# Kernel tuning notes

Measured on AMD Instinct MI355X. Metric: run time of the kernel, lower is better.

Reference implementation:

```python
import jax, jax.numpy as jnp
import numpy as np

B, NE, NMAX = 256, 90, 270
ZE = PE = GE = PPS = 32
NPROPS = 20
FP, SGE, LATH = 256, 64, 128
PIN = FP + SGE + LATH  # 448 = pred_inp_size = conv input (add_to_node)
C1, C2, H = 448, 256, 3
P1 = P2 = 512
EPS = 1e-5

PNAMES = ['sg_emb_table','lat_W1','lat_b1','lat_bn1_g','lat_bn1_b','lat_bn1_m','lat_bn1_v',
          'lat_W2','lat_b2','lat_bn2_g','lat_bn2_b','lat_bn2_m','lat_bn2_v',
          'z_emb_table','period_table','group_table','props','W_props','b_props','W_phys','b_phys',
          'gat1_W','gat1_as','gat1_ad','gat1_b','gat2_W','gat2_as','gat2_ad','gat2_b',
          'pW1','pb1','pbn1_g','pbn1_b','pbn1_m','pbn1_v',
          'pW2','pb2','pbn2_g','pbn2_b','pbn2_m','pbn2_v','pW3','pb3']

def _bn(x, g, b, m, v):
    return (x - m) * g / jnp.sqrt(v + EPS) + b

def _lrelu(x, s=0.2):
    return jnp.where(x >= 0, x, s * x)

def _gat(x, adj, W, a_s, a_d, bias):
    # PyG DenseGATConv: concat=False (mean over heads), dropout=0, negative_slope=0.2
    Bn, N, _ = x.shape
    h = (x @ W).reshape(Bn, N, H, -1)                      # [B,N,H,C]
    asrc = (h * a_s).sum(-1)                               # [B,N,H]
    adst = (h * a_d).sum(-1)
    alpha = asrc[:, None, :, :] + adst[:, :, None, :]      # [B,i,j,H]
    alpha = _lrelu(alpha, 0.2)
    adj_sl = jnp.maximum(adj, jnp.eye(N, dtype=adj.dtype))  # add self loops
    alpha = jnp.where(adj_sl[..., None] > 0, alpha, -jnp.inf)
    alpha = jax.nn.softmax(alpha, axis=2)                  # softmax over sources j
    out = jnp.einsum('bijh,bjhc->bihc', alpha, h)
    return out.mean(2) + bias                              # [B,N,C]

def _forward(comp, sg, lat, period_idx, group_idx, p):
    sg_x = p['sg_emb_table'][sg[:, 0]]                     # [B,SGE]
    # lattice MLP: (Linear -> BN -> LeakyReLU(True)==identity) x2
    h = _bn(lat @ p['lat_W1'] + p['lat_b1'], p['lat_bn1_g'], p['lat_bn1_b'], p['lat_bn1_m'], p['lat_bn1_v'])
    lat_x = _bn(h @ p['lat_W2'] + p['lat_b2'], p['lat_bn2_g'], p['lat_bn2_b'], p['lat_bn2_m'], p['lat_bn2_v'])
    # ragged -> dense batch: expand composition counts into dense node-type grid
    n_atoms = comp.sum(1)                                  # [B]
    cum = jnp.cumsum(comp, axis=1)                         # [B,NE]
    t = jnp.arange(NMAX)
    z = jax.vmap(lambda c: jnp.searchsorted(c, t, side='right'))(cum)  # [B,NMAX]
    mask = t[None, :] < n_atoms[:, None]                   # [B,NMAX] valid nodes
    z = jnp.where(mask, z, 0)
    # PhysEmbedding: z/period/group embeddings + projected properties -> final proj
    phys = jnp.concatenate([
        p['z_emb_table'][z],
        p['period_table'][period_idx[z]],
        p['group_table'][group_idx[z]],
        p['props'][z] @ p['W_props'] + p['b_props'],
    ], axis=-1)
    phys = phys @ p['W_phys'] + p['b_phys']                # [B,NMAX,FP]
    # add_to_node: cat graph-level lat/sg embeddings onto every node, then zero-pad
    node = jnp.concatenate([
        phys,
        jnp.broadcast_to(lat_x[:, None, :], (lat_x.shape[0], NMAX, LATH)),
        jnp.broadcast_to(sg_x[:, None, :], (sg_x.shape[0], NMAX, SGE)),
    ], axis=-1)
    node = node * mask[..., None].astype(node.dtype)       # to_dense_batch zero padding
    # per-graph dense block adjacency, zero diagonal (fill_diagonal_(0))
    adj = (mask[:, :, None] & mask[:, None, :]).astype(node.dtype)
    adj = adj * (1.0 - jnp.eye(NMAX, dtype=node.dtype))
    # GNNBlock: act = LeakyReLU(True) == identity (negative_slope=1)
    x1 = _gat(node, adj, p['gat1_W'], p['gat1_as'], p['gat1_ad'], p['gat1_b'])
    x2 = _gat(x1, adj, p['gat2_W'], p['gat2_as'], p['gat2_ad'], p['gat2_b'])
    comp_x = x2.sum(1)                                     # sum over ALL NMAX slots (incl. padding, as torch does)
    feat = jnp.concatenate([comp_x, sg_x, lat_x], axis=-1) # [B,PIN]
    # prediction head (eval: dropout off, BN running stats)
    h = _lrelu(_bn(feat @ p['pW1'] + p['pb1'], p['pbn1_g'], p['pbn1_b'], p['pbn1_m'], p['pbn1_v']))
    h = _lrelu(_bn(h @ p['pW2'] + p['pb2'], p['pbn2_g'], p['pbn2_b'], p['pbn2_m'], p['pbn2_v']))
    return h @ p['pW3'] + p['pb3']                         # [B,1]

def setup_inputs():
    key = jax.random.key(0)
    ks = iter(jax.random.split(key, 64))
    def nrm(shape, s=0.05):
        return jax.random.normal(next(ks), shape, dtype=jnp.float32) * s
    comp = jax.random.randint(next(ks), (B, NE), 0, 4, dtype=jnp.int32)
    comp = comp.at[0].set(3)  # graph 0 has exactly NMAX atoms -> data N_max == NMAX
    sg = jax.random.randint(next(ks), (B, 1), 0, 230)
    lat = jax.random.uniform(next(ks), (B, 6), dtype=jnp.float32)
    period_idx = jax.random.randint(next(ks), (NE,), 0, 8)
    group_idx = jax.random.randint(next(ks), (NE,), 0, 19)
    inp = dict(comp=comp, sg=sg, lat=lat, period_idx=period_idx, group_idx=group_idx)
    inp.update(
        sg_emb_table=nrm((230, SGE)),
        lat_W1=nrm((6, LATH)), lat_b1=nrm((LATH,)),
        lat_bn1_g=jnp.ones(LATH), lat_bn1_b=jnp.zeros(LATH), lat_bn1_m=jnp.zeros(LATH), lat_bn1_v=jnp.ones(LATH),
        lat_W2=nrm((LATH, LATH)), lat_b2=nrm((LATH,)),
        lat_bn2_g=jnp.ones(LATH), lat_bn2_b=jnp.zeros(LATH), lat_bn2_m=jnp.zeros(LATH), lat_bn2_v=jnp.ones(LATH),
        z_emb_table=nrm((NE, ZE)), period_table=nrm((8, PE)), group_table=nrm((19, GE)),
        props=nrm((NE, NPROPS), 0.1), W_props=nrm((NPROPS, PPS)), b_props=nrm((PPS,)),
        W_phys=nrm((ZE + PE + GE + PPS, FP)), b_phys=nrm((FP,)),
        gat1_W=nrm((PIN, H * C1)), gat1_as=nrm((H, C1)), gat1_ad=nrm((H, C1)), gat1_b=nrm((C1,)),
        gat2_W=nrm((C1, H * C2)), gat2_as=nrm((H, C2)), gat2_ad=nrm((H, C2)), gat2_b=nrm((C2,)),
        pW1=nrm((PIN, P1)), pb1=nrm((P1,)),
        pbn1_g=jnp.ones(P1), pbn1_b=jnp.zeros(P1), pbn1_m=jnp.zeros(P1), pbn1_v=jnp.ones(P1),
        pW2=nrm((P1, P2)), pb2=nrm((P2,)),
        pbn2_g=jnp.ones(P2), pbn2_b=jnp.zeros(P2), pbn2_m=jnp.zeros(P2), pbn2_v=jnp.ones(P2),
        pW3=nrm((P2, 1)), pb3=nrm((1,)),
    )
    return inp

def reference(comp, sg, lat, period_idx, group_idx,
              sg_emb_table, lat_W1, lat_b1, lat_bn1_g, lat_bn1_b, lat_bn1_m, lat_bn1_v,
              lat_W2, lat_b2, lat_bn2_g, lat_bn2_b, lat_bn2_m, lat_bn2_v,
              z_emb_table, period_table, group_table, props, W_props, b_props, W_phys, b_phys,
              gat1_W, gat1_as, gat1_ad, gat1_b, gat2_W, gat2_as, gat2_ad, gat2_b,
              pW1, pb1, pbn1_g, pbn1_b, pbn1_m, pbn1_v,
              pW2, pb2, pbn2_g, pbn2_b, pbn2_m, pbn2_v, pW3, pb3):
    vals = (sg_emb_table, lat_W1, lat_b1, lat_bn1_g, lat_bn1_b, lat_bn1_m, lat_bn1_v,
            lat_W2, lat_b2, lat_bn2_g, lat_bn2_b, lat_bn2_m, lat_bn2_v,
            z_emb_table, period_table, group_table, props, W_props, b_props, W_phys, b_phys,
            gat1_W, gat1_as, gat1_ad, gat1_b, gat2_W, gat2_as, gat2_ad, gat2_b,
            pW1, pb1, pbn1_g, pbn1_b, pbn1_m, pbn1_v,
            pW2, pb2, pbn2_g, pbn2_b, pbn2_m, pbn2_v, pW3, pb3)
    p = dict(zip(PNAMES, vals))
    return _forward(comp, sg, lat, period_idx, group_idx, p)
```

## Files before the change

kernel.cpp:

```cpp
#include <hip/hip_runtime.h>
#include <math.h>

#define BB 256
#define NEL 90
#define NMAX 270
#define C1 448
#define C2 256
#define PIN 448
#define LATH 128
#define SGE 64
#define P1 512
#define EPSB 1e-5f

typedef short shortx8 __attribute__((ext_vector_type(8)));
typedef float floatx4 __attribute__((ext_vector_type(4)));

__device__ __forceinline__ float bf2f(unsigned short u) {
  return __uint_as_float(((unsigned)u) << 16);
}
__device__ __forceinline__ unsigned short f2bf(float f) {
  unsigned x = __float_as_uint(f);
  unsigned r = (x + 0x7fffu + ((x >> 16) & 1u)) >> 16;
  return (unsigned short)r;
}
__device__ __forceinline__ void gld16(const void* g, void* l) {
  __builtin_amdgcn_global_load_lds(
      (const __attribute__((address_space(1))) unsigned int*)g,
      (__attribute__((address_space(3))) unsigned int*)l, 16, 0, 0);
}

#define NB_PREP  BB
#define NB_SCAN  1
#define NB_PHYS  NEL
#define NB_WP1   (14 * 42)
#define NB_WP2   (14 * 24)
#define NB_FOLD  112
#define NB_PAD   64
#define SETUP_GRID (NB_PREP + NB_SCAN + NB_PHYS + NB_WP1 + NB_WP2 + 2 * NB_FOLD + NB_PAD)

__global__ __launch_bounds__(256) void k_setup(
    const int* __restrict__ comp, const int* __restrict__ sg, const float* __restrict__ lat,
    const float* __restrict__ sg_emb,
    const float* __restrict__ lW1, const float* __restrict__ lb1,
    const float* __restrict__ lg1, const float* __restrict__ lbe1,
    const float* __restrict__ lm1, const float* __restrict__ lv1,
    const float* __restrict__ lW2, const float* __restrict__ lb2,
    const float* __restrict__ lg2, const float* __restrict__ lbe2,
    const float* __restrict__ lm2, const float* __restrict__ lv2,
    const int* __restrict__ period_idx, const int* __restrict__ group_idx,
    const float* __restrict__ z_emb, const float* __restrict__ period_t,
    const float* __restrict__ group_t, const float* __restrict__ props,
    const float* __restrict__ Wp, const float* __restrict__ bp,
    const float* __restrict__ Wphys, const float* __restrict__ bphys,
    const float* __restrict__ gat1_W, const float* __restrict__ gat1_as,
    const float* __restrict__ gat1_ad, const float* __restrict__ gat1_b,
    const float* __restrict__ gat2_W, const float* __restrict__ gat2_as,
    const float* __restrict__ gat2_ad, const float* __restrict__ gat2_b,
    float* __restrict__ sgx, float* __restrict__ latx, int* __restrict__ z,
    int* __restrict__ natoms, int* __restrict__ off, int* __restrict__ aoff,
    float* __restrict__ zerobuf, float* __restrict__ physpe,
    unsigned short* __restrict__ wt1, unsigned short* __restrict__ wt2,
    float* __restrict__ wsv1, float* __restrict__ wdv1,
    float* __restrict__ wsv2, float* __restrict__ wdv2, float* __restrict__ pad2) {
  int r = blockIdx.x;
  int tid = threadIdx.x;
  int wv = tid >> 6, lane = tid & 63;

  if (r < NB_PREP) {
    int b = r;
    __shared__ int cum[NEL];
    __shared__ float hbuf[LATH];
    __shared__ float latl[6];
    if (tid == 0) {
      int s = 0;
      for (int e = 0; e < NEL; ++e) { s += comp[b * NEL + e]; cum[e] = s; }
    }
    if (tid < 6) latl[tid] = lat[b * 6 + tid];
    __syncthreads();
    int n = cum[NEL - 1];
    for (int t = tid; t < NMAX; t += 256) {
      int zz = -1;
      if (t < n) {
        for (int e = 0; e < NEL; ++e) { if (cum[e] > t) { zz = e; break; } }
      }
      z[b * NMAX + t] = zz;
    }
    if (tid < SGE) sgx[b * SGE + tid] = sg_emb[sg[b] * SGE + tid];
    if (tid < LATH) {
      float acc = lb1[tid];
      for (int k = 0; k < 6; ++k) acc += latl[k] * lW1[k * LATH + tid];
      acc = (acc - lm1[tid]) * lg1[tid] * rsqrtf(lv1[tid] + EPSB) + lbe1[tid];
      hbuf[tid] = acc;
    }
    __syncthreads();
    if (tid < LATH) {
      float acc = lb2[tid];
      for (int k = 0; k < LATH; ++k) acc += hbuf[k] * lW2[k * LATH + tid];
      acc = (acc - lm2[tid]) * lg2[tid] * rsqrtf(lv2[tid] + EPSB) + lbe2[tid];
      latx[b * LATH + tid] = acc;
    }
    return;
  }
  r -= NB_PREP;
  if (r < NB_SCAN) {
    __shared__ int sh[BB];
    zerobuf[tid] = 0.f;
    int v0 = 0;
    for (int e = 0; e < NEL; ++e) v0 += comp[tid * NEL + e];
    natoms[tid] = v0;
    sh[tid] = v0;
    for (int d = 1; d < BB; d <<= 1) {
      __syncthreads();
      int v = (tid >= d) ? sh[tid - d] : 0;
      __syncthreads();
      sh[tid] += v;
    }
    __syncthreads();
    off[tid] = sh[tid] - v0;
    __syncthreads();
    int sz = 3 * ((((v0 + 15) >> 4) << 4)) * ((((v0 + 31) >> 5) << 5));
    sh[tid] = sz;
    for (int d = 1; d < BB; d <<= 1) {
      __syncthreads();
      int v = (tid >= d) ? sh[tid - d] : 0;
      __syncthreads();
      sh[tid] += v;
    }
    __syncthreads();
    aoff[tid] = sh[tid] - sz;
    return;
  }
  r -= NB_SCAN;
  if (r < NB_PHYS) {
    int e = r;
    __shared__ float ph[128];
    if (tid < 32) ph[tid] = z_emb[e * 32 + tid];
    else if (tid < 64) ph[tid] = period_t[period_idx[e] * 32 + tid - 32];
    else if (tid < 96) ph[tid] = group_t[group_idx[e] * 32 + tid - 64];
    else if (tid < 128) {
      int j = tid - 96;
      float acc = bp[j];
      for (int k = 0; k < 20; ++k) acc += props[e * 20 + k] * Wp[k * 32 + j];
      ph[tid] = acc;
    }
    __syncthreads();
    float acc = bphys[tid];
    for (int k = 0; k < 128; ++k) acc += ph[k] * Wphys[k * 256 + tid];
    physpe[e * 256 + tid] = acc;
    return;
  }
  r -= NB_PHYS;
  if (r < NB_WP1 + NB_WP2) {
    const float* W;
    unsigned short* Wt;
    int NC3, bx, by;
    if (r < NB_WP1) { W = gat1_W; Wt = wt1; NC3 = 3 * C1; bx = r % 14; by = r / 14; }
    else { int r2 = r - NB_WP1; W = gat2_W; Wt = wt2; NC3 = 3 * C2; bx = r2 % 14; by = r2 / 14; }
    int k0 = bx << 5, c0 = by << 5;
    __shared__ float ts[32][33];
    int e4 = tid << 2;
    int kk = e4 >> 5, cc = e4 & 31;
    float4 v = *(const float4*)(W + (size_t)(k0 + kk) * NC3 + c0 + cc);
    ts[kk][cc] = v.x; ts[kk][cc + 1] = v.y; ts[kk][cc + 2] = v.z; ts[kk][cc + 3] = v.w;
    __syncthreads();
    int c2 = tid & 31, kg = tid >> 5;
    ushort4 u;
    u.x = f2bf(ts[kg * 4 + 0][c2]); u.y = f2bf(ts[kg * 4 + 1][c2]);
    u.z = f2bf(ts[kg * 4 + 2][c2]); u.w = f2bf(ts[kg * 4 + 3][c2]);
    *(ushort4*)(Wt + (size_t)(c0 + c2) * 448 + k0 + (kg << 2)) = u;
    return;
  }
  r -= NB_WP1 + NB_WP2;
  if (r < 2 * NB_FOLD) {
    const float* W; const float* as_; const float* ad_;
    float* wsv; float* wdv; int NC3, C, kb;
    if (r < NB_FOLD) { W = gat1_W; as_ = gat1_as; ad_ = gat1_ad; wsv = wsv1; wdv = wdv1; NC3 = 3 * C1; C = C1; kb = r << 2; }
    else { int r2 = r - NB_FOLD; W = gat2_W; as_ = gat2_as; ad_ = gat2_ad; wsv = wsv2; wdv = wdv2; NC3 = 3 * C2; C = C2; kb = r2 << 2; }
    int k = kb + wv;
    for (int h = 0; h < 3; ++h) {
      float ss = 0.f, sd = 0.f;
      for (int c = lane; c < C; c += 64) {
        float wvv = W[(size_t)k * NC3 + h * C + c];
        ss += wvv * as_[h * C + c];
        sd += wvv * ad_[h * C + c];
      }
      for (int o = 32; o > 0; o >>= 1) { ss += __shfl_xor(ss, o); sd += __shfl_xor(sd, o); }
      if (lane == 0) { wsv[k * 3 + h] = ss; wdv[k * 3 + h] = sd; }
    }
    return;
  }
  r -= 2 * NB_FOLD;
  {
    int c = (r << 2) + wv;
    float s = 0.f;
    for (int k = lane; k < C1; k += 64) {
      const float* wr = gat2_W + (size_t)k * (3 * C2) + c;
      s += gat1_b[k] * (wr[0] + wr[C2] + wr[2 * C2]);
    }
    for (int o = 32; o > 0; o >>= 1) s += __shfl_xor(s, o);
    if (lane == 0) pad2[c] = s * (1.f / 3.f) + gat2_b[c];
  }
}

__global__ __launch_bounds__(256) void k_nodep(
    const int* __restrict__ z, const int* __restrict__ off, const int* __restrict__ natoms,
    const float* __restrict__ physpe, const float* __restrict__ latx,
    const float* __restrict__ sgx, unsigned short* __restrict__ x0) {
  int b = blockIdx.x;
  int n = natoms[b], ob = off[b];
  int tid = threadIdx.x;
  __shared__ int zl[NMAX];
  for (int t = tid; t < n; t += 256) zl[t] = z[b * NMAX + t];
  __syncthreads();
  int items = n * 56;
  for (int e = tid; e < items; e += 256) {
    int t = e / 56, c8 = (e - t * 56) << 3;
    int zt = zl[t];
    float v[8];
    if (c8 < 256) {
      float4 a = *(const float4*)(physpe + zt * 256 + c8);
      float4 c = *(const float4*)(physpe + zt * 256 + c8 + 4);
      v[0] = a.x; v[1] = a.y; v[2] = a.z; v[3] = a.w;
      v[4] = c.x; v[5] = c.y; v[6] = c.z; v[7] = c.w;
    } else if (c8 < 384) {
      float4 a = *(const float4*)(latx + b * LATH + c8 - 256);
      float4 c = *(const float4*)(latx + b * LATH + c8 - 252);
      v[0] = a.x; v[1] = a.y; v[2] = a.z; v[3] = a.w;
      v[4] = c.x; v[5] = c.y; v[6] = c.z; v[7] = c.w;
    } else {
      float4 a = *(const float4*)(sgx + b * SGE + c8 - 384);
      float4 c = *(const float4*)(sgx + b * SGE + c8 - 380);
      v[0] = a.x; v[1] = a.y; v[2] = a.z; v[3] = a.w;
      v[4] = c.x; v[5] = c.y; v[6] = c.z; v[7] = c.w;
    }
    unsigned short u[8];
    #pragma unroll
    for (int i = 0; i < 8; ++i) u[i] = f2bf(v[i]);
    *(uint4*)(x0 + (size_t)(ob + t) * PIN + c8) = *(uint4*)u;
  }
}

__global__ __launch_bounds__(256) void k_av2(
    const unsigned short* __restrict__ x, const float* __restrict__ wsv,
    const float* __restrict__ wdv, const int* __restrict__ off,
    const int* __restrict__ natoms, float* __restrict__ asrc,
    float* __restrict__ adst, int K) {
  __shared__ float sw[C1 * 3], dw[C1 * 3];
  int tid = threadIdx.x;
  for (int e = tid; e < K * 3; e += 256) { sw[e] = wsv[e]; dw[e] = wdv[e]; }
  __syncthreads();
  int total = off[BB - 1] + natoms[BB - 1];
  int wv = tid >> 6, lane = tid & 63;
  int nk8 = K >> 3;
  int stride = gridDim.x << 2;
  for (int row = (blockIdx.x << 2) + wv; row < total; row += stride) {
    float s0 = 0.f, s1 = 0.f, s2 = 0.f, d0 = 0.f, d1 = 0.f, d2 = 0.f;
    if (lane < nk8) {
      uint4 raw = *(const uint4*)(x + (size_t)row * K + (lane << 3));
      unsigned short us[8];
      *(uint4*)us = raw;
      #pragma unroll
      for (int u = 0; u < 8; ++u) {
        float xv = bf2f(us[u]);
        int kb = ((lane << 3) + u) * 3;
        s0 += xv * sw[kb + 0]; s1 += xv * sw[kb + 1]; s2 += xv * sw[kb + 2];
        d0 += xv * dw[kb + 0]; d1 += xv * dw[kb + 1]; d2 += xv * dw[kb + 2];
      }
    }
    #pragma unroll
    for (int o = 32; o > 0; o >>= 1) {
      s0 += __shfl_xor(s0, o); s1 += __shfl_xor(s1, o); s2 += __shfl_xor(s2, o);
      d0 += __shfl_xor(d0, o); d1 += __shfl_xor(d1, o); d2 += __shfl_xor(d2, o);
    }
    if (lane == 0) {
      asrc[row * 3 + 0] = s0; asrc[row * 3 + 1] = s1; asrc[row * 3 + 2] = s2;
      adst[row * 3 + 0] = d0; adst[row * 3 + 1] = d1; adst[row * 3 + 2] = d2;
    }
  }
}

#define MTMAX 17
__global__ __launch_bounds__(256) void k_alpha(
    const float* __restrict__ asrc, const float* __restrict__ adst,
    const int* __restrict__ off, const int* __restrict__ natoms,
    const int* __restrict__ aoff, unsigned short* __restrict__ alpha) {
  int bid = blockIdx.x;
  int b = bid & (BB - 1);
  int hm = bid >> 8;
  int h = hm % 3;
  int mt = hm / 3;
  int n = natoms[b];
  if (n == 0) return;
  int mtn = (n + 15) >> 4;
  if (mt >= mtn) return;
  int ktn = (n + 31) >> 5;
  int rext = mtn << 4, kext = ktn << 5;
  int ob = off[b];
  size_t ab = (size_t)aoff[b] + (size_t)h * rext * kext;
  int tid = threadIdx.x;
  int wv = tid >> 6, lane = tid & 63;
  __shared__ float asl[288];
  for (int j = tid; j < kext; j += 256)
    asl[j] = (j < n) ? asrc[(ob + j) * 3 + h] : 0.f;
  __syncthreads();
  #pragma unroll
  for (int r = 0; r < 4; ++r) {
    int i = (mt << 4) + (wv << 2) + r;
    unsigned short* rowp = alpha + ab + (size_t)i * kext;
    if (i >= n) {
      for (int j = lane; j < kext; j += 64) rowp[j] = 0;
      continue;
    }
    float ad = adst[(ob + i) * 3 + h];
    float m = -1e30f;
    for (int j = lane; j < n; j += 64) {
      float sc = asl[j] + ad;
      sc = fmaxf(sc, 0.2f * sc);
      m = fmaxf(m, sc);
    }
    for (int o = 32; o > 0; o >>= 1) m = fmaxf(m, __shfl_xor(m, o));
    float s = 0.f;
    for (int j = lane; j < n; j += 64) {
      float sc = asl[j] + ad;
      sc = fmaxf(sc, 0.2f * sc);
      s += __expf(sc - m);
    }
    for (int o = 32; o > 0; o >>= 1) s += __shfl_xor(s, o);
    float rs = 1.f / s;
    for (int j = lane; j < kext; j += 64) {
      float v = 0.f;
      if (j < n) {
        float sc = asl[j] + ad;
        sc = fmaxf(sc, 0.2f * sc);
        v = __expf(sc - m) * rs;
      }
      rowp[j] = f2bf(v);
    }
  }
}

#define MTW 5

__global__ __launch_bounds__(256, 2) void k_fused_mfma(
    const unsigned short* __restrict__ xin, const unsigned short* __restrict__ Wt,
    const unsigned short* __restrict__ alpha, const int* __restrict__ aoff,
    const int* __restrict__ off, const int* __restrict__ natoms,
    const float* __restrict__ bias, const float* __restrict__ zerobuf,
    unsigned short* __restrict__ xout, int K, int C, int NC) {
  int bid = blockIdx.x;
  int xg = bid & 7;
  int g = bid >> 3;
  int cblk = g % NC;
  int b = xg + ((g / NC) << 3);
  int c0 = cblk << 6;
  int n = natoms[b];
  if (n == 0) return;
  int ob = off[b];
  size_t ab = (size_t)aoff[b];
  int tid = threadIdx.x;
  int wv = tid >> 6;
  int lane = tid & 63;
  int m16 = lane & 15;
  int q = lane >> 4;

  int mtn = (n + 15) >> 4;
  int jmax = mtn << 4;
  int ktn = (n + 31) >> 5;
  int kext = ktn << 5;
  size_t hstride = (size_t)jmax * kext;

  __shared__ unsigned short xs[2][17 * 512];
  __shared__ unsigned short tt[36 * 512];

  const unsigned short* xsrc[MTW];
  #pragma unroll
  for (int t_i = 0; t_i < MTW; ++t_i) {
    int mt = wv + (t_i << 2);
    int j = (mt << 4) + m16;
    xsrc[t_i] = (j < n) ? (xin + (size_t)(ob + j) * K + (q << 3))
                        : (const unsigned short*)zerobuf;
  }

  floatx4 acc[MTW][4];
  #pragma unroll
  for (int i = 0; i < MTW; ++i)
    #pragma unroll
    for (int nt = 0; nt < 4; ++nt) acc[i][nt] = (floatx4)0.f;

  for (int h = 0; h < 3; ++h) {
    floatx4 tac[MTW][4];
    #pragma unroll
    for (int i = 0; i < MTW; ++i)
      #pragma unroll
      for (int nt = 0; nt < 4; ++nt) tac[i][nt] = (floatx4)0.f;

    const unsigned short* wsrc = Wt + (size_t)(h * C + c0 + lane) * K + (wv << 3);

    #pragma unroll
    for (int t_i = 0; t_i < MTW; ++t_i) {
      int mt = wv + (t_i << 2);
      if (mt < mtn) gld16(xsrc[t_i], &xs[0][mt << 9]);
    }
    gld16(wsrc, &tt[wv << 9]);
    __syncthreads();

    int buf = 0;
    for (int k0 = 0; k0 < K; k0 += 32) {
      int k1 = k0 + 32;
      if (k1 < K) {
        #pragma unroll
        for (int t_i = 0; t_i < MTW; ++t_i) {
          int mt = wv + (t_i << 2);
          if (mt < mtn) gld16(xsrc[t_i] + k1, &xs[buf ^ 1][mt << 9]);
        }
        gld16(wsrc + k1, &tt[((buf ^ 1) << 11) + (wv << 9)]);
      }
      const unsigned short* wb = &tt[buf << 11];
      shortx8 bfr[4];
      #pragma unroll
      for (int nt = 0; nt < 4; ++nt)
        bfr[nt] = *(const shortx8*)(wb + (q << 9) + (((nt << 4) + m16) << 3));
      #pragma unroll
      for (int t_i = 0; t_i < MTW; ++t_i) {
        int mt = wv + (t_i << 2);
        if (mt < mtn) {
          shortx8 a = *(const shortx8*)(&xs[buf][(mt << 9) + (((q << 4) + m16) << 3)]);
          #pragma unroll
          for (int nt = 0; nt < 4; ++nt)
            tac[t_i][nt] = __builtin_amdgcn_mfma_f32_16x16x32_bf16(a, bfr[nt], tac[t_i][nt], 0, 0, 0);
        }
      }
      __syncthreads();
      buf ^= 1;
    }
    #pragma unroll
    for (int t_i = 0; t_i < MTW; ++t_i) {
      int mt = wv + (t_i << 2);
      if (mt < mtn) {
        int jbase = (mt << 4) + (q << 2);
        #pragma unroll
        for (int nt = 0; nt < 4; ++nt) {
          floatx4 d = tac[t_i][nt];
          ushort4 u;
          u.x = f2bf(d.x); u.y = f2bf(d.y); u.z = f2bf(d.z); u.w = f2bf(d.w);
          int c = (nt << 4) + m16;
          *(ushort4*)(tt + ((jbase >> 3) << 9) + (c << 3) + (jbase & 7)) = u;
        }
      }
    }
    for (int e = tid; e < ((kext - jmax) << 6); e += 256) {
      int j = jmax + (e >> 6), c = e & 63;
      tt[((j >> 3) << 9) + (c << 3) + (j & 7)] = 0;
    }
    __syncthreads();
    const unsigned short* ap = alpha + ab + (size_t)h * hstride;
    for (int k0p = 0; k0p < kext; k0p += 32) {
      shortx8 tb[4];
      #pragma unroll
      for (int nt = 0; nt < 4; ++nt)
        tb[nt] = *(const shortx8*)(tt + (((k0p >> 3) + q) << 9) + (((nt << 4) + m16) << 3));
      #pragma unroll
      for (int t_i = 0; t_i < MTW; ++t_i) {
        int mt = wv + (t_i << 2);
        if (mt < mtn) {
          shortx8 af = *(const shortx8*)(ap + (size_t)((mt << 4) + m16) * kext + k0p + (q << 3));
          #pragma unroll
          for (int nt = 0; nt < 4; ++nt)
            acc[t_i][nt] = __builtin_amdgcn_mfma_f32_16x16x32_bf16(af, tb[nt], acc[t_i][nt], 0, 0, 0);
        }
      }
    }
    __syncthreads();
  }
  float bq[4];
  #pragma unroll
  for (int nt = 0; nt < 4; ++nt) bq[nt] = bias[c0 + (nt << 4) + m16];
  const float inv3 = 1.f / 3.f;
  #pragma unroll
  for (int t_i = 0; t_i < MTW; ++t_i) {
    int mt = wv + (t_i << 2);
    if (mt < mtn) {
      #pragma unroll
      for (int nt = 0; nt < 4; ++nt) {
        floatx4 d = acc[t_i][nt];
        int cidx = c0 + (nt << 4) + m16;
        #pragma unroll
        for (int r = 0; r < 4; ++r) {
          int i = (mt << 4) + (q << 2) + r;
          if (i < n) xout[(size_t)(ob + i) * C + cidx] = f2bf(d[r] * inv3 + bq[nt]);
        }
      }
    }
  }
}

__global__ __launch_bounds__(256) void k_feat2(
    const unsigned short* __restrict__ x2, const float* __restrict__ pad2,
    const int* __restrict__ off, const int* __restrict__ natoms,
    const float* __restrict__ sgx, const float* __restrict__ latx,
    float* __restrict__ feat) {
  int b = blockIdx.y;
  int chunk = blockIdx.x;
  int tid = threadIdx.x;
  int n = natoms[b], ob = off[b];
  if (chunk == 17) {
    atomicAdd(&feat[b * PIN + tid], (float)(NMAX - n) * pad2[tid]);
    if (tid < SGE) feat[b * PIN + 256 + tid] = sgx[b * SGE + tid];
    if (tid < LATH) feat[b * PIN + 320 + tid] = latx[b * LATH + tid];
    return;
  }
  int i0 = chunk << 4;
  if (i0 >= n) return;
  int i1 = min(i0 + 16, n);
  float s = 0.f;
  for (int i = i0; i < i1; ++i) s += bf2f(x2[(size_t)(ob + i) * C2 + tid]);
  atomicAdd(&feat[b * PIN + tid], s);
}

__global__ __launch_bounds__(512) void k_head(
    const float* __restrict__ feat,
    const float* __restrict__ W1, const float* __restrict__ b1,
    const float* __restrict__ g1, const float* __restrict__ be1,
    const float* __restrict__ m1, const float* __restrict__ v1,
    const float* __restrict__ W2, const float* __restrict__ b2,
    const float* __restrict__ g2, const float* __restrict__ be2,
    const float* __restrict__ m2, const float* __restrict__ v2,
    const float* __restrict__ W3, const float* __restrict__ b3,
    float* __restrict__ out) {
  int b = blockIdx.x, tid = threadIdx.x;
  __shared__ float f[PIN];
  __shared__ float h1[P1];
  __shared__ float h2[P1];
  __shared__ float red[512];
  for (int i = tid; i < PIN; i += 512) f[i] = feat[b * PIN + i];
  __syncthreads();
  {
    int o = tid;
    float acc = b1[o];
    for (int k = 0; k < PIN; ++k) acc += f[k] * W1[k * P1 + o];
    acc = (acc - m1[o]) * g1[o] * rsqrtf(v1[o] + EPSB) + be1[o];
    h1[o] = acc >= 0.f ? acc : 0.2f * acc;
  }
  __syncthreads();
  {
    int o = tid;
    float acc = b2[o];
    for (int k = 0; k < P1; ++k) acc += h1[k] * W2[k * P1 + o];
    acc = (acc - m2[o]) * g2[o] * rsqrtf(v2[o] + EPSB) + be2[o];
    h2[o] = acc >= 0.f ? acc : 0.2f * acc;
  }
  __syncthreads();
  red[tid] = h2[tid] * W3[tid];
  __syncthreads();
  for (int s = 256; s > 0; s >>= 1) {
    if (tid < s) red[tid] += red[tid + s];
    __syncthreads();
  }
  if (tid == 0) out[b] = red[0] + b3[0];
}

extern "C" void kernel_launch(void* const* d_in, const int* in_sizes, int n_in,
                              void* d_out, int out_size, void* d_ws, size_t ws_size,
                              hipStream_t stream) {
  const int*   comp       = (const int*)d_in[0];
  const int*   sg         = (const int*)d_in[1];
  const float* lat        = (const float*)d_in[2];
  const int*   period_idx = (const int*)d_in[3];
  const int*   group_idx  = (const int*)d_in[4];
  const float* sg_emb     = (const float*)d_in[5];
  const float* lat_W1     = (const float*)d_in[6];
  const float* lat_b1     = (const float*)d_in[7];
  const float* lat_bn1_g  = (const float*)d_in[8];
  const float* lat_bn1_b  = (const float*)d_in[9];
  const float* lat_bn1_m  = (const float*)d_in[10];
  const float* lat_bn1_v  = (const float*)d_in[11];
  const float* lat_W2     = (const float*)d_in[12];
  const float* lat_b2     = (const float*)d_in[13];
  const float* lat_bn2_g  = (const float*)d_in[14];
  const float* lat_bn2_b  = (const float*)d_in[15];
  const float* lat_bn2_m  = (const float*)d_in[16];
  const float* lat_bn2_v  = (const float*)d_in[17];
  const float* z_emb      = (const float*)d_in[18];
  const float* period_t   = (const float*)d_in[19];
  const float* group_t    = (const float*)d_in[20];
  const float* props      = (const float*)d_in[21];
  const float* W_props    = (const float*)d_in[22];
  const float* b_props    = (const float*)d_in[23];
  const float* W_phys     = (const float*)d_in[24];
  const float* b_phys     = (const float*)d_in[25];
  const float* gat1_W     = (const float*)d_in[26];
  const float* gat1_as    = (const float*)d_in[27];
  const float* gat1_ad    = (const float*)d_in[28];
  const float* gat1_b     = (const float*)d_in[29];
  const float* gat2_W     = (const float*)d_in[30];
  const float* gat2_as    = (const float*)d_in[31];
  const float* gat2_ad    = (const float*)d_in[32];
  const float* gat2_b     = (const float*)d_in[33];
  const float* pW1        = (const float*)d_in[34];
  const float* pb1        = (const float*)d_in[35];
  const float* pbn1_g     = (const float*)d_in[36];
  const float* pbn1_b     = (const float*)d_in[37];
  const float* pbn1_m     = (const float*)d_in[38];
  const float* pbn1_v     = (const float*)d_in[39];
  const float* pW2        = (const float*)d_in[40];
  const float* pb2        = (const float*)d_in[41];
  const float* pbn2_g     = (const float*)d_in[42];
  const float* pbn2_b     = (const float*)d_in[43];
  const float* pbn2_m     = (const float*)d_in[44];
  const float* pbn2_v     = (const float*)d_in[45];
  const float* pW3        = (const float*)d_in[46];
  const float* pb3        = (const float*)d_in[47];

  float* ws = (float*)d_ws;
  const size_t o_sgx  = 0;
  const size_t o_latx = o_sgx  + (size_t)BB * SGE;
  const size_t o_nat  = o_latx + (size_t)BB * LATH;
  const size_t o_off  = o_nat  + BB;
  const size_t o_aoff = o_off  + BB;
  const size_t o_z    = o_aoff + BB;
  const size_t o_phys = o_z    + (size_t)BB * NMAX;
  const size_t o_wsv1 = o_phys + (size_t)NEL * 256;
  const size_t o_wdv1 = o_wsv1 + (size_t)C1 * 3;
  const size_t o_wsv2 = o_wdv1 + (size_t)C1 * 3;
  const size_t o_wdv2 = o_wsv2 + (size_t)C1 * 3;
  const size_t o_asrc = o_wdv2 + (size_t)C1 * 3;
  const size_t o_adst = o_asrc + (size_t)BB * NMAX * 3;
  const size_t o_pad2 = o_adst + (size_t)BB * NMAX * 3;
  const size_t o_zero = o_pad2 + 256;
  const size_t o_wt1  = o_zero + 256;
  const size_t o_wt2  = o_wt1  + (size_t)(3 * C1) * PIN / 2;
  const size_t o_x0   = o_wt2  + (size_t)(3 * C2) * C1 / 2;
  const size_t o_x1   = o_x0   + (size_t)BB * NMAX * PIN / 2;
  const size_t o_alph = o_x1   + (size_t)BB * NMAX * PIN / 2;

  float* sgx    = ws + o_sgx;
  float* latx   = ws + o_latx;
  int*   natoms = (int*)(ws + o_nat);
  int*   off    = (int*)(ws + o_off);
  int*   aoff   = (int*)(ws + o_aoff);
  int*   z      = (int*)(ws + o_z);
  float* physpe = ws + o_phys;
  float* wsv1   = ws + o_wsv1;
  float* wdv1   = ws + o_wdv1;
  float* wsv2   = ws + o_wsv2;
  float* wdv2   = ws + o_wdv2;
  float* asrc   = ws + o_asrc;
  float* adst   = ws + o_adst;
  float* pad2   = ws + o_pad2;
  float* zerobuf = ws + o_zero;
  unsigned short* wt1   = (unsigned short*)(ws + o_wt1);
  unsigned short* wt2   = (unsigned short*)(ws + o_wt2);
  unsigned short* x0    = (unsigned short*)(ws + o_x0);
  unsigned short* x1    = (unsigned short*)(ws + o_x1);
  unsigned short* x2    = x0;
  unsigned short* alpha = (unsigned short*)(ws + o_alph);
  float* feat   = ws + o_x1;

  const int ALG = BB * 3 * MTMAX;

  k_setup<<<SETUP_GRID, 256, 0, stream>>>(
      comp, sg, lat, sg_emb,
      lat_W1, lat_b1, lat_bn1_g, lat_bn1_b, lat_bn1_m, lat_bn1_v,
      lat_W2, lat_b2, lat_bn2_g, lat_bn2_b, lat_bn2_m, lat_bn2_v,
      period_idx, group_idx, z_emb, period_t, group_t, props,
      W_props, b_props, W_phys, b_phys,
      gat1_W, gat1_as, gat1_ad, gat1_b,
      gat2_W, gat2_as, gat2_ad, gat2_b,
      sgx, latx, z, natoms, off, aoff, zerobuf, physpe,
      wt1, wt2, wsv1, wdv1, wsv2, wdv2, pad2);

  k_nodep<<<BB, 256, 0, stream>>>(z, off, natoms, physpe, latx, sgx, x0);

  k_av2<<<1024, 256, 0, stream>>>(x0, wsv1, wdv1, off, natoms, asrc, adst, PIN);
  k_alpha<<<ALG, 256, 0, stream>>>(asrc, adst, off, natoms, aoff, alpha);
  k_fused_mfma<<<(C1 / 64) * BB, 256, 0, stream>>>(x0, wt1, alpha, aoff,
      off, natoms, gat1_b, zerobuf, x1, PIN, C1, C1 / 64);

  k_av2<<<1024, 256, 0, stream>>>(x1, wsv2, wdv2, off, natoms, asrc, adst, C1);
  k_alpha<<<ALG, 256, 0, stream>>>(asrc, adst, off, natoms, aoff, alpha);
  k_fused_mfma<<<(C2 / 64) * BB, 256, 0, stream>>>(x1, wt2, alpha, aoff,
      off, natoms, gat2_b, zerobuf, x2, C1, C2, C2 / 64);

  hipMemsetAsync(feat, 0, (size_t)BB * PIN * sizeof(float), stream);
  k_feat2<<<dim3(18, BB), 256, 0, stream>>>(x2, pad2, off, natoms, sgx, latx, feat);
  k_head<<<BB, 512, 0, stream>>>(feat,
      pW1, pb1, pbn1_g, pbn1_b, pbn1_m, pbn1_v,
      pW2, pb2, pbn2_g, pbn2_b, pbn2_m, pbn2_v,
      pW3, pb3, (float*)d_out);
}
```

Baseline: 747.0 us.

## Fuse node build, attention scores and softmax per graph; fuse pooling into head

Node feature construction, the attention-vector dot products and the softmax alpha computation are merged into one per-graph kernel that keeps asrc/adst in shared memory. The same merge is done for layer two. Feature pooling is folded into the MLP head, which removes the memset, the atomics and the feat buffer. Launches and global round-trips go down, but each stage now runs on only 256 blocks, so GPU occupancy is lower. Layer one's attention scores now use the fp32 features instead of the bf16-rounded ones.

```diff
diff --git a/kernel.cpp b/kernel.cpp
--- a/kernel.cpp
+++ b/kernel.cpp
@@ -202,126 +202,29 @@
   }
 }
 
-__global__ __launch_bounds__(256) void k_nodep(
-    const int* __restrict__ z, const int* __restrict__ off, const int* __restrict__ natoms,
-    const float* __restrict__ physpe, const float* __restrict__ latx,
-    const float* __restrict__ sgx, unsigned short* __restrict__ x0) {
-  int b = blockIdx.x;
-  int n = natoms[b], ob = off[b];
-  int tid = threadIdx.x;
-  __shared__ int zl[NMAX];
-  for (int t = tid; t < n; t += 256) zl[t] = z[b * NMAX + t];
-  __syncthreads();
-  int items = n * 56;
-  for (int e = tid; e < items; e += 256) {
-    int t = e / 56, c8 = (e - t * 56) << 3;
-    int zt = zl[t];
-    float v[8];
-    if (c8 < 256) {
-      float4 a = *(const float4*)(physpe + zt * 256 + c8);
-      float4 c = *(const float4*)(physpe + zt * 256 + c8 + 4);
-      v[0] = a.x; v[1] = a.y; v[2] = a.z; v[3] = a.w;
-      v[4] = c.x; v[5] = c.y; v[6] = c.z; v[7] = c.w;
-    } else if (c8 < 384) {
-      float4 a = *(const float4*)(latx + b * LATH + c8 - 256);
-      float4 c = *(const float4*)(latx + b * LATH + c8 - 252);
-      v[0] = a.x; v[1] = a.y; v[2] = a.z; v[3] = a.w;
-      v[4] = c.x; v[5] = c.y; v[6] = c.z; v[7] = c.w;
-    } else {
-      float4 a = *(const float4*)(sgx + b * SGE + c8 - 384);
-      float4 c = *(const float4*)(sgx + b * SGE + c8 - 380);
-      v[0] = a.x; v[1] = a.y; v[2] = a.z; v[3] = a.w;
-      v[4] = c.x; v[5] = c.y; v[6] = c.z; v[7] = c.w;
-    }
-    unsigned short u[8];
-    #pragma unroll
-    for (int i = 0; i < 8; ++i) u[i] = f2bf(v[i]);
-    *(uint4*)(x0 + (size_t)(ob + t) * PIN + c8) = *(uint4*)u;
-  }
-}
-
-__global__ __launch_bounds__(256) void k_av2(
-    const unsigned short* __restrict__ x, const float* __restrict__ wsv,
-    const float* __restrict__ wdv, const int* __restrict__ off,
-    const int* __restrict__ natoms, float* __restrict__ asrc,
-    float* __restrict__ adst, int K) {
-  __shared__ float sw[C1 * 3], dw[C1 * 3];
-  int tid = threadIdx.x;
-  for (int e = tid; e < K * 3; e += 256) { sw[e] = wsv[e]; dw[e] = wdv[e]; }
-  __syncthreads();
-  int total = off[BB - 1] + natoms[BB - 1];
-  int wv = tid >> 6, lane = tid & 63;
-  int nk8 = K >> 3;
-  int stride = gridDim.x << 2;
-  for (int row = (blockIdx.x << 2) + wv; row < total; row += stride) {
-    float s0 = 0.f, s1 = 0.f, s2 = 0.f, d0 = 0.f, d1 = 0.f, d2 = 0.f;
-    if (lane < nk8) {
-      uint4 raw = *(const uint4*)(x + (size_t)row * K + (lane << 3));
-      unsigned short us[8];
-      *(uint4*)us = raw;
-      #pragma unroll
-      for (int u = 0; u < 8; ++u) {
-        float xv = bf2f(us[u]);
-        int kb = ((lane << 3) + u) * 3;
-        s0 += xv * sw[kb + 0]; s1 += xv * sw[kb + 1]; s2 += xv * sw[kb + 2];
-        d0 += xv * dw[kb + 0]; d1 += xv * dw[kb + 1]; d2 += xv * dw[kb + 2];
-      }
-    }
-    #pragma unroll
-    for (int o = 32; o > 0; o >>= 1) {
-      s0 += __shfl_xor(s0, o); s1 += __shfl_xor(s1, o); s2 += __shfl_xor(s2, o);
-      d0 += __shfl_xor(d0, o); d1 += __shfl_xor(d1, o); d2 += __shfl_xor(d2, o);
-    }
-    if (lane == 0) {
-      asrc[row * 3 + 0] = s0; asrc[row * 3 + 1] = s1; asrc[row * 3 + 2] = s2;
-      adst[row * 3 + 0] = d0; adst[row * 3 + 1] = d1; adst[row * 3 + 2] = d2;
-    }
-  }
-}
-
-#define MTMAX 17
-__global__ __launch_bounds__(256) void k_alpha(
-    const float* __restrict__ asrc, const float* __restrict__ adst,
-    const int* __restrict__ off, const int* __restrict__ natoms,
-    const int* __restrict__ aoff, unsigned short* __restrict__ alpha) {
-  int bid = blockIdx.x;
-  int b = bid & (BB - 1);
-  int hm = bid >> 8;
-  int h = hm % 3;
-  int mt = hm / 3;
-  int n = natoms[b];
-  if (n == 0) return;
-  int mtn = (n + 15) >> 4;
-  if (mt >= mtn) return;
-  int ktn = (n + 31) >> 5;
-  int rext = mtn << 4, kext = ktn << 5;
-  int ob = off[b];
-  size_t ab = (size_t)aoff[b] + (size_t)h * rext * kext;
-  int tid = threadIdx.x;
-  int wv = tid >> 6, lane = tid & 63;
-  __shared__ float asl[288];
-  for (int j = tid; j < kext; j += 256)
-    asl[j] = (j < n) ? asrc[(ob + j) * 3 + h] : 0.f;
-  __syncthreads();
-  #pragma unroll
-  for (int r = 0; r < 4; ++r) {
-    int i = (mt << 4) + (wv << 2) + r;
-    unsigned short* rowp = alpha + ab + (size_t)i * kext;
+__device__ __forceinline__ void alpha_phase(
+    const float* asl, const float* adl, unsigned short* __restrict__ alpha,
+    size_t ab, int n, int rext, int kext, int wv8, int lane) {
+  for (int hr = wv8; hr < 3 * rext; hr += 8) {
+    int h = (hr >= 2 * rext) ? 2 : (hr >= rext ? 1 : 0);
+    int i = hr - h * rext;
+    unsigned short* rowp = alpha + ab + (size_t)h * rext * kext + (size_t)i * kext;
     if (i >= n) {
       for (int j = lane; j < kext; j += 64) rowp[j] = 0;
       continue;
     }
-    float ad = adst[(ob + i) * 3 + h];
+    const float* asp = asl + h * 288;
+    float ad = adl[h * 288 + i];
     float m = -1e30f;
     for (int j = lane; j < n; j += 64) {
-      float sc = asl[j] + ad;
+      float sc = asp[j] + ad;
       sc = fmaxf(sc, 0.2f * sc);
       m = fmaxf(m, sc);
     }
     for (int o = 32; o > 0; o >>= 1) m = fmaxf(m, __shfl_xor(m, o));
     float s = 0.f;
     for (int j = lane; j < n; j += 64) {
-      float sc = asl[j] + ad;
+      float sc = asp[j] + ad;
       sc = fmaxf(sc, 0.2f * sc);
       s += __expf(sc - m);
     }
@@ -330,13 +233,128 @@
     for (int j = lane; j < kext; j += 64) {
       float v = 0.f;
       if (j < n) {
-        float sc = asl[j] + ad;
+        float sc = asp[j] + ad;
         sc = fmaxf(sc, 0.2f * sc);
         v = __expf(sc - m) * rs;
       }
       rowp[j] = f2bf(v);
     }
   }
+}
+
+__global__ __launch_bounds__(512) void k_node_avalpha(
+    const int* __restrict__ z, const int* __restrict__ off, const int* __restrict__ natoms,
+    const float* __restrict__ physpe, const float* __restrict__ latx,
+    const float* __restrict__ sgx, const float* __restrict__ wsv,
+    const float* __restrict__ wdv, const int* __restrict__ aoff,
+    unsigned short* __restrict__ x0, unsigned short* __restrict__ alpha) {
+  int b = blockIdx.x;
+  int n = natoms[b];
+  if (n == 0) return;
+  int ob = off[b];
+  int tid = threadIdx.x;
+  int wv8 = tid >> 6, lane = tid & 63;
+  __shared__ int zl[NMAX];
+  __shared__ float wsl[PIN * 3], wdl[PIN * 3];
+  __shared__ float asl[3 * 288], adl[3 * 288];
+  for (int t = tid; t < n; t += 512) zl[t] = z[b * NMAX + t];
+  for (int e = tid; e < PIN * 3; e += 512) { wsl[e] = wsv[e]; wdl[e] = wdv[e]; }
+  for (int e = tid; e < 3 * 288; e += 512) { asl[e] = 0.f; adl[e] = 0.f; }
+  __syncthreads();
+  int mtn = (n + 15) >> 4, ktn = (n + 31) >> 5;
+  int rext = mtn << 4, kext = ktn << 5;
+  for (int r = wv8; r < n; r += 8) {
+    int zt = zl[r];
+    float s0 = 0.f, s1 = 0.f, s2 = 0.f, d0 = 0.f, d1 = 0.f, d2 = 0.f;
+    if (lane < 56) {
+      int c8 = lane << 3;
+      float v[8];
+      if (c8 < 256) {
+        float4 a = *(const float4*)(physpe + zt * 256 + c8);
+        float4 c = *(const float4*)(physpe + zt * 256 + c8 + 4);
+        v[0] = a.x; v[1] = a.y; v[2] = a.z; v[3] = a.w;
+        v[4] = c.x; v[5] = c.y; v[6] = c.z; v[7] = c.w;
+      } else if (c8 < 384) {
+        float4 a = *(const float4*)(latx + b * LATH + c8 - 256);
+        float4 c = *(const float4*)(latx + b * LATH + c8 - 252);
+        v[0] = a.x; v[1] = a.y; v[2] = a.z; v[3] = a.w;
+        v[4] = c.x; v[5] = c.y; v[6] = c.z; v[7] = c.w;
+      } else {
+        float4 a = *(const float4*)(sgx + b * SGE + c8 - 384);
+        float4 c = *(const float4*)(sgx + b * SGE + c8 - 380);
+        v[0] = a.x; v[1] = a.y; v[2] = a.z; v[3] = a.w;
+        v[4] = c.x; v[5] = c.y; v[6] = c.z; v[7] = c.w;
+      }
+      unsigned short u[8];
+      #pragma unroll
+      for (int i = 0; i < 8; ++i) u[i] = f2bf(v[i]);
+      *(uint4*)(x0 + (size_t)(ob + r) * PIN + c8) = *(uint4*)u;
+      #pragma unroll
+      for (int i = 0; i < 8; ++i) {
+        int kb = (c8 + i) * 3;
+        s0 += v[i] * wsl[kb + 0]; s1 += v[i] * wsl[kb + 1]; s2 += v[i] * wsl[kb + 2];
+        d0 += v[i] * wdl[kb + 0]; d1 += v[i] * wdl[kb + 1]; d2 += v[i] * wdl[kb + 2];
+      }
+    }
+    #pragma unroll
+    for (int o = 32; o > 0; o >>= 1) {
+      s0 += __shfl_xor(s0, o); s1 += __shfl_xor(s1, o); s2 += __shfl_xor(s2, o);
+      d0 += __shfl_xor(d0, o); d1 += __shfl_xor(d1, o); d2 += __shfl_xor(d2, o);
+    }
+    if (lane == 0) {
+      asl[0 * 288 + r] = s0; asl[1 * 288 + r] = s1; asl[2 * 288 + r] = s2;
+      adl[0 * 288 + r] = d0; adl[1 * 288 + r] = d1; adl[2 * 288 + r] = d2;
+    }
+  }
+  __syncthreads();
+  alpha_phase(asl, adl, alpha, (size_t)aoff[b], n, rext, kext, wv8, lane);
+}
+
+__global__ __launch_bounds__(512) void k_avalpha(
+    const unsigned short* __restrict__ x, const float* __restrict__ wsv,
+    const float* __restrict__ wdv, const int* __restrict__ off,
+    const int* __restrict__ natoms, const int* __restrict__ aoff,
+    unsigned short* __restrict__ alpha) {
+  int b = blockIdx.x;
+  int n = natoms[b];
+  if (n == 0) return;
+  int ob = off[b];
+  int tid = threadIdx.x;
+  int wv8 = tid >> 6, lane = tid & 63;
+  __shared__ float wsl[C1 * 3], wdl[C1 * 3];
+  __shared__ float asl[3 * 288], adl[3 * 288];
+  for (int e = tid; e < C1 * 3; e += 512) { wsl[e] = wsv[e]; wdl[e] = wdv[e]; }
+  for (int e = tid; e < 3 * 288; e += 512) { asl[e] = 0.f; adl[e] = 0.f; }
+  __syncthreads();
+  int mtn = (n + 15) >> 4, ktn = (n + 31) >> 5;
+  int rext = mtn << 4, kext = ktn << 5;
+  for (int r = wv8; r < n; r += 8) {
+    float s0 = 0.f, s1 = 0.f, s2 = 0.f, d0 = 0.f, d1 = 0.f, d2 = 0.f;
+    if (lane < 56) {
+      int c8 = lane << 3;
+      uint4 raw = *(const uint4*)(x + (size_t)(ob + r) * C1 + c8);
+      unsigned short us[8];
+      *(uint4*)us = raw;
+      #pragma unroll
+      for (int i = 0; i < 8; ++i) {
+        float v = bf2f(us[i]);
+        int kb = (c8 + i) * 3;
+        s0 += v * wsl[kb + 0]; s1 += v * wsl[kb + 1]; s2 += v * wsl[kb + 2];
+        d0 += v * wdl[kb + 0]; d1 += v * wdl[kb + 1]; d2 += v * wdl[kb + 2];
+      }
+    }
+    #pragma unroll
+    for (int o = 32; o > 0; o >>= 1) {
+      s0 += __shfl_xor(s0, o); s1 += __shfl_xor(s1, o); s2 += __shfl_xor(s2, o);
+      d0 += __shfl_xor(d0, o); d1 += __shfl_xor(d1, o); d2 += __shfl_xor(d2, o);
+    }
+    if (lane == 0) {
+      asl[0 * 288 + r] = s0; asl[1 * 288 + r] = s1; asl[2 * 288 + r] = s2;
+      adl[0 * 288 + r] = d0; adl[1 * 288 + r] = d1; adl[2 * 288 + r] = d2;
+    }
+  }
+  __syncthreads();
+  alpha_phase(asl, adl, alpha, (size_t)aoff[b], n, rext, kext, wv8, lane);
 }
 
 #define MTW 5
@@ -494,31 +512,10 @@
   }
 }
 
-__global__ __launch_bounds__(256) void k_feat2(
+__global__ __launch_bounds__(512) void k_feat_head(
     const unsigned short* __restrict__ x2, const float* __restrict__ pad2,
     const int* __restrict__ off, const int* __restrict__ natoms,
     const float* __restrict__ sgx, const float* __restrict__ latx,
-    float* __restrict__ feat) {
-  int b = blockIdx.y;
-  int chunk = blockIdx.x;
-  int tid = threadIdx.x;
-  int n = natoms[b], ob = off[b];
-  if (chunk == 17) {
-    atomicAdd(&feat[b * PIN + tid], (float)(NMAX - n) * pad2[tid]);
-    if (tid < SGE) feat[b * PIN + 256 + tid] = sgx[b * SGE + tid];
-    if (tid < LATH) feat[b * PIN + 320 + tid] = latx[b * LATH + tid];
-    return;
-  }
-  int i0 = chunk << 4;
-  if (i0 >= n) return;
-  int i1 = min(i0 + 16, n);
-  float s = 0.f;
-  for (int i = i0; i < i1; ++i) s += bf2f(x2[(size_t)(ob + i) * C2 + tid]);
-  atomicAdd(&feat[b * PIN + tid], s);
-}
-
-__global__ __launch_bounds__(512) void k_head(
-    const float* __restrict__ feat,
     const float* __restrict__ W1, const float* __restrict__ b1,
     const float* __restrict__ g1, const float* __restrict__ be1,
     const float* __restrict__ m1, const float* __restrict__ v1,
@@ -528,11 +525,35 @@
     const float* __restrict__ W3, const float* __restrict__ b3,
     float* __restrict__ out) {
   int b = blockIdx.x, tid = threadIdx.x;
+  int wv8 = tid >> 6, lane = tid & 63;
+  int n = natoms[b], ob = off[b];
+  __shared__ float part[8][256];
   __shared__ float f[PIN];
   __shared__ float h1[P1];
   __shared__ float h2[P1];
   __shared__ float red[512];
-  for (int i = tid; i < PIN; i += 512) f[i] = feat[b * PIN + i];
+  float a0 = 0.f, a1 = 0.f, a2 = 0.f, a3 = 0.f;
+  for (int r = wv8; r < n; r += 8) {
+    uint2 raw = *(const uint2*)(x2 + (size_t)(ob + r) * C2 + (lane << 2));
+    unsigned short us[4];
+    *(uint2*)us = raw;
+    a0 += bf2f(us[0]); a1 += bf2f(us[1]); a2 += bf2f(us[2]); a3 += bf2f(us[3]);
+  }
+  {
+    float4 p = make_float4(a0, a1, a2, a3);
+    *(float4*)&part[wv8][lane << 2] = p;
+  }
+  __syncthreads();
+  if (tid < 256) {
+    float s = 0.f;
+    #pragma unroll
+    for (int w = 0; w < 8; ++w) s += part[w][tid];
+    f[tid] = s + (float)(NMAX - n) * pad2[tid];
+  } else if (tid < 320) {
+    f[tid] = sgx[b * SGE + (tid - 256)];
+  } else if (tid < 448) {
+    f[tid] = latx[b * LATH + (tid - 320)];
+  }
   __syncthreads();
   {
     int o = tid;
@@ -623,9 +644,7 @@
   const size_t o_wdv1 = o_wsv1 + (size_t)C1 * 3;
   const size_t o_wsv2 = o_wdv1 + (size_t)C1 * 3;
   const size_t o_wdv2 = o_wsv2 + (size_t)C1 * 3;
-  const size_t o_asrc = o_wdv2 + (size_t)C1 * 3;
-  const size_t o_adst = o_asrc + (size_t)BB * NMAX * 3;
-  const size_t o_pad2 = o_adst + (size_t)BB * NMAX * 3;
+  const size_t o_pad2 = o_wdv2 + (size_t)C1 * 3;
   const size_t o_zero = o_pad2 + 256;
   const size_t o_wt1  = o_zero + 256;
   const size_t o_wt2  = o_wt1  + (size_t)(3 * C1) * PIN / 2;
@@ -644,8 +663,6 @@
   float* wdv1   = ws + o_wdv1;
   float* wsv2   = ws + o_wsv2;
   float* wdv2   = ws + o_wdv2;
-  float* asrc   = ws + o_asrc;
-  float* adst   = ws + o_adst;
   float* pad2   = ws + o_pad2;
   float* zerobuf = ws + o_zero;
   unsigned short* wt1   = (unsigned short*)(ws + o_wt1);
@@ -654,9 +671,6 @@
   unsigned short* x1    = (unsigned short*)(ws + o_x1);
   unsigned short* x2    = x0;
   unsigned short* alpha = (unsigned short*)(ws + o_alph);
-  float* feat   = ws + o_x1;
-
-  const int ALG = BB * 3 * MTMAX;
 
   k_setup<<<SETUP_GRID, 256, 0, stream>>>(
       comp, sg, lat, sg_emb,
@@ -669,21 +683,18 @@
       sgx, latx, z, natoms, off, aoff, zerobuf, physpe,
       wt1, wt2, wsv1, wdv1, wsv2, wdv2, pad2);
 
-  k_nodep<<<BB, 256, 0, stream>>>(z, off, natoms, physpe, latx, sgx, x0);
-
-  k_av2<<<1024, 256, 0, stream>>>(x0, wsv1, wdv1, off, natoms, asrc, adst, PIN);
-  k_alpha<<<ALG, 256, 0, stream>>>(asrc, adst, off, natoms, aoff, alpha);
+  k_node_avalpha<<<BB, 512, 0, stream>>>(z, off, natoms, physpe, latx, sgx,
+      wsv1, wdv1, aoff, x0, alpha);
+
   k_fused_mfma<<<(C1 / 64) * BB, 256, 0, stream>>>(x0, wt1, alpha, aoff,
       off, natoms, gat1_b, zerobuf, x1, PIN, C1, C1 / 64);
 
-  k_av2<<<1024, 256, 0, stream>>>(x1, wsv2, wdv2, off, natoms, asrc, adst, C1);
-  k_alpha<<<ALG, 256, 0, stream>>>(asrc, adst, off, natoms, aoff, alpha);
+  k_avalpha<<<BB, 512, 0, stream>>>(x1, wsv2, wdv2, off, natoms, aoff, alpha);
+
   k_fused_mfma<<<(C2 / 64) * BB, 256, 0, stream>>>(x1, wt2, alpha, aoff,
       off, natoms, gat2_b, zerobuf, x2, C1, C2, C2 / 64);
 
-  hipMemsetAsync(feat, 0, (size_t)BB * PIN * sizeof(float), stream);
-  k_feat2<<<dim3(18, BB), 256, 0, stream>>>(x2, pad2, off, natoms, sgx, latx, feat);
-  k_head<<<BB, 512, 0, stream>>>(feat,
+  k_feat_head<<<BB, 512, 0, stream>>>(x2, pad2, off, natoms, sgx, latx,
       pW1, pb1, pbn1_g, pbn1_b, pbn1_m, pbn1_v,
       pW2, pb2, pbn2_g, pbn2_b, pbn2_m, pbn2_v,
       pW3, pb3, (float*)d_out);
```

Result: slower. 1.010 ms (+35.2%).
